# Optimization experiments

Hardware: AMD Instinct MI355X
Metric: run time of the kernel (lower is better)

Reference implementation:

```python
import jax, jax.numpy as jnp
import numpy as np

N_NODES = 50000
N_EDGES = 800000
NFEAT, NHID, NCLASS = 256, 64, 40


def setup_inputs() -> dict:
    key = jax.random.key(0)
    ks = jax.random.split(key, 8)
    x = jax.random.normal(ks[0], (N_NODES, NFEAT), dtype=jnp.float32)
    W1 = jax.random.normal(ks[1], (NFEAT, NHID), dtype=jnp.float32) * (1.0 / np.sqrt(NFEAT))
    b1 = jax.random.normal(ks[2], (NHID,), dtype=jnp.float32) * 0.01
    W2 = jax.random.normal(ks[3], (NHID, NCLASS), dtype=jnp.float32) * (1.0 / np.sqrt(NHID))
    b2 = jax.random.normal(ks[4], (NCLASS,), dtype=jnp.float32) * 0.01
    edge_weight = jax.random.uniform(ks[5], (N_EDGES,), dtype=jnp.float32)
    edge_src = jax.random.randint(ks[6], (N_EDGES,), 0, N_NODES)
    edge_dst = jax.random.randint(ks[7], (N_EDGES,), 0, N_NODES)
    return {"x": x, "W1": W1, "b1": b1, "W2": W2, "b2": b2,
            "edge_weight": edge_weight, "edge_src": edge_src, "edge_dst": edge_dst}


def reference(x, W1, b1, W2, b2, edge_weight, edge_src, edge_dst):
    n = x.shape[0]

    def spmm(h):  # sparse adj @ h via gather + weighted segment-sum
        msgs = h[edge_src] * edge_weight[:, None]  # [E, d]
        return jax.ops.segment_sum(msgs, edge_dst, num_segments=n)

    # gc1: adj @ (x @ W1) + b1, then relu (dropout is identity in eval mode)
    h = jax.nn.relu(spmm(x @ W1) + b1)
    # gc2: adj @ (h @ W2) + b2
    logits = spmm(h @ W2) + b2
    return (logits, jax.nn.log_softmax(logits, axis=1))
```

## Files before the change

### kernel.cpp

```cpp
#include <hip/hip_runtime.h>
#include <math.h>

#define N_NODES 50000
#define N_EDGES 800000
#define NFEAT 256
#define NHID 64
#define NCLASS 40
#define NPB 16
#define NB  3125
#define CAP 512
#define BIN_EPB 8192
#define NBIN 98
#define NGEMM 782
#define ACC2S 68

typedef __attribute__((ext_vector_type(8))) short bf16x8;
typedef __attribute__((ext_vector_type(4))) float f32x4;

__device__ __forceinline__ ushort f2bf(float f) {
    unsigned u = __float_as_uint(f);
    u += 0x7FFF + ((u >> 16) & 1);
    return (ushort)(u >> 16);
}
__device__ __forceinline__ float bf2f(ushort us) {
    return __uint_as_float(((unsigned)us) << 16);
}

__global__ __launch_bounds__(256) void k_prep(const float* __restrict__ W1,
                                              const float* __restrict__ W2,
                                              ushort* __restrict__ W1f,
                                              ushort* __restrict__ W2f) {
    int idx = blockIdx.x * 256 + threadIdx.x;
    if (idx < 2048) {
        int lane = idx & 63, ctks = idx >> 6;
        int ks = ctks & 7, ct = ctks >> 3;
        int col = ct * 16 + (lane & 15);
        int r0 = ks * 32 + (lane >> 4) * 8;
        bf16x8 frag;
        #pragma unroll
        for (int j = 0; j < 8; ++j) frag[j] = (short)f2bf(W1[(r0 + j) * NHID + col]);
        *(bf16x8*)&W1f[(size_t)idx * 8] = frag;
    } else if (idx < 2048 + 384) {
        int i2 = idx - 2048;
        int lane = i2 & 63, ctks = i2 >> 6;
        int ks = ctks & 1, ct = ctks >> 1;
        int col = ct * 16 + (lane & 15);
        int r0 = ks * 32 + (lane >> 4) * 8;
        bf16x8 frag;
        #pragma unroll
        for (int j = 0; j < 8; ++j)
            frag[j] = (short)((col < NCLASS) ? f2bf(W2[(r0 + j) * NCLASS + col]) : 0);
        *(bf16x8*)&W2f[(size_t)i2 * 8] = frag;
    }
}

__global__ __launch_bounds__(1024) void k_mega(const int* __restrict__ esrc,
                                               const int* __restrict__ edst,
                                               const float* __restrict__ ewt,
                                               int* __restrict__ bfill,
                                               int2* __restrict__ binned,
                                               const float* __restrict__ x,
                                               const ushort* __restrict__ W1f,
                                               ushort* __restrict__ xW1b) {
    __shared__ __align__(16) char smem[64 * 256 * 2];
    int tid = threadIdx.x;

    if (blockIdx.x < NBIN) {
        int* lcnt  = (int*)smem;
        int* lbase = lcnt + NB;
        for (int i = tid; i < NB; i += 1024) lcnt[i] = 0;
        __syncthreads();
        int base = blockIdx.x * BIN_EPB;
        #pragma unroll
        for (int k = 0; k < BIN_EPB; k += 1024) {
            int e = base + k + tid;
            if (e < N_EDGES) atomicAdd(&lcnt[edst[e] >> 4], 1);
        }
        __syncthreads();
        for (int i = tid; i < NB; i += 1024) {
            int c = lcnt[i];
            lbase[i] = c ? atomicAdd(&bfill[i], c) : 0;
            lcnt[i] = 0;
        }
        __syncthreads();
        #pragma unroll
        for (int k = 0; k < BIN_EPB; k += 1024) {
            int e = base + k + tid;
            if (e < N_EDGES) {
                int d = edst[e];
                int b = d >> 4;
                int pos = b * CAP + lbase[b] + atomicAdd(&lcnt[b], 1);
                binned[pos] = make_int2(esrc[e] | ((d & 15) << 16),
                                        __float_as_int(ewt[e]));
            }
        }
        return;
    }

    ushort* sX = (ushort*)smem;
    int w = tid >> 6, lane = tid & 63;
    int ct = w & 3, rg = w >> 2;
    int row0 = (blockIdx.x - NBIN) * 64;

    bf16x8 Bf[8];
    #pragma unroll
    for (int ks = 0; ks < 8; ++ks)
        Bf[ks] = *(const bf16x8*)&W1f[(size_t)((ct * 8 + ks) * 64 + lane) * 8];

    {
        int row = tid & 63;
        int colbase = (tid >> 6) * 16;
        int crow = min(row0 + row, N_NODES - 1);
        const float* xp = x + (size_t)crow * NFEAT + colbase;
        #pragma unroll
        for (int c2 = 0; c2 < 2; ++c2) {
            float4 v0 = *(const float4*)(xp + c2 * 8);
            float4 v1 = *(const float4*)(xp + c2 * 8 + 4);
            bf16x8 fr;
            fr[0] = (short)f2bf(v0.x); fr[1] = (short)f2bf(v0.y);
            fr[2] = (short)f2bf(v0.z); fr[3] = (short)f2bf(v0.w);
            fr[4] = (short)f2bf(v1.x); fr[5] = (short)f2bf(v1.y);
            fr[6] = (short)f2bf(v1.z); fr[7] = (short)f2bf(v1.w);
            int chunk = colbase / 8 + c2;
            *(bf16x8*)&sX[row * 256 + ((chunk ^ (row & 7)) * 8)] = fr;
        }
    }
    __syncthreads();

    f32x4 acc = {0.f, 0.f, 0.f, 0.f};
    int arow = rg * 16 + (lane & 15);
    #pragma unroll
    for (int ks = 0; ks < 8; ++ks) {
        int chunk = ks * 4 + (lane >> 4);
        bf16x8 Af = *(const bf16x8*)&sX[arow * 256 + ((chunk ^ (arow & 7)) * 8)];
        acc = __builtin_amdgcn_mfma_f32_16x16x32_bf16(Af, Bf[ks], acc, 0, 0, 0);
    }
    int col = ct * 16 + (lane & 15);
    int rbase = row0 + rg * 16 + (lane >> 4) * 4;
    #pragma unroll
    for (int r = 0; r < 4; ++r) {
        int row = rbase + r;
        if (row < N_NODES)
            xW1b[(size_t)row * NHID + col] = f2bf(acc[r]);
    }
}

__global__ __launch_bounds__(256) void k_spmm1b(const ushort* __restrict__ xW1b,
                                                const int* __restrict__ bfill,
                                                const int2* __restrict__ binned,
                                                const float* __restrict__ b1,
                                                ushort* __restrict__ h_b) {
    __shared__ float accs[4][NPB * NHID];
    int wv = threadIdx.x >> 6, lane = threadIdx.x & 63;
    int b = blockIdx.x;
    float* acc = accs[wv];
    #pragma unroll
    for (int n = 0; n < NPB; ++n) acc[n * NHID + lane] = 0.f;

    int s = b * CAP, e = s + bfill[b];
    int len = e - s;
    int q = (len + 3) >> 2;
    int j = s + wv * q;
    int je = min(j + q, e);
    for (; j + 8 <= je; j += 8) {
        int2 p[8];
        #pragma unroll
        for (int k = 0; k < 8; ++k) p[k] = binned[j + k];
        float g[8];
        #pragma unroll
        for (int k = 0; k < 8; ++k)
            g[k] = bf2f(xW1b[(p[k].x & 0xFFFF) * NHID + lane]);
        #pragma unroll
        for (int k = 0; k < 8; ++k)
            acc[(p[k].x >> 16) * NHID + lane] += __int_as_float(p[k].y) * g[k];
    }
    for (; j < je; ++j) {
        int2 p0 = binned[j];
        float g0 = bf2f(xW1b[(p0.x & 0xFFFF) * NHID + lane]);
        acc[(p0.x >> 16) * NHID + lane] += __int_as_float(p0.y) * g0;
    }
    __syncthreads();

    float bias = b1[lane];
    #pragma unroll
    for (int i = 0; i < 4; ++i) {
        int n = wv * 4 + i;
        float v = accs[0][n * NHID + lane] + accs[1][n * NHID + lane]
                + accs[2][n * NHID + lane] + accs[3][n * NHID + lane] + bias;
        h_b[(size_t)(b * NPB + n) * NHID + lane] = f2bf(v > 0.f ? v : 0.f);
    }
}

__global__ __launch_bounds__(256) void k_spmm2f(const ushort* __restrict__ h_b,
                                                const int* __restrict__ bfill,
                                                const int2* __restrict__ binned,
                                                const ushort* __restrict__ W2f,
                                                const float* __restrict__ b2,
                                                float* __restrict__ out) {
    __shared__ float accs[4][NPB * ACC2S];
    int wv = threadIdx.x >> 6, lane = threadIdx.x & 63;
    int b = blockIdx.x;
    float* acc = accs[wv];
    #pragma unroll
    for (int n = 0; n < NPB; ++n) acc[n * ACC2S + lane] = 0.f;

    int s = b * CAP, e = s + bfill[b];
    int len = e - s;
    int q = (len + 3) >> 2;
    int j = s + wv * q;
    int je = min(j + q, e);
    for (; j + 8 <= je; j += 8) {
        int2 p[8];
        #pragma unroll
        for (int k = 0; k < 8; ++k) p[k] = binned[j + k];
        float g[8];
        #pragma unroll
        for (int k = 0; k < 8; ++k)
            g[k] = bf2f(h_b[(p[k].x & 0xFFFF) * NHID + lane]);
        #pragma unroll
        for (int k = 0; k < 8; ++k)
            acc[(p[k].x >> 16) * ACC2S + lane] += __int_as_float(p[k].y) * g[k];
    }
    for (; j < je; ++j) {
        int2 p0 = binned[j];
        float g0 = bf2f(h_b[(p0.x & 0xFFFF) * NHID + lane]);
        acc[(p0.x >> 16) * ACC2S + lane] += __int_as_float(p0.y) * g0;
    }
    __syncthreads();

    for (int i = threadIdx.x; i < NPB * 64; i += 256) {
        int idx = (i >> 6) * ACC2S + (i & 63);
        accs[0][idx] = accs[0][idx] + accs[1][idx] + accs[2][idx] + accs[3][idx];
    }
    __syncthreads();
    if (wv != 0) return;

    bf16x8 Af[2];
    #pragma unroll
    for (int ks = 0; ks < 2; ++ks) {
        const float* ap = &accs[0][(lane & 15) * ACC2S + ks * 32 + (lane >> 4) * 8];
        #pragma unroll
        for (int jj = 0; jj < 8; ++jj) Af[ks][jj] = (short)f2bf(ap[jj]);
    }
    f32x4 cv[3] = {{0.f,0.f,0.f,0.f},{0.f,0.f,0.f,0.f},{0.f,0.f,0.f,0.f}};
    #pragma unroll
    for (int ct = 0; ct < 3; ++ct) {
        #pragma unroll
        for (int ks = 0; ks < 2; ++ks) {
            bf16x8 Bf = *(const bf16x8*)&W2f[(size_t)((ct * 2 + ks) * 64 + lane) * 8];
            cv[ct] = __builtin_amdgcn_mfma_f32_16x16x32_bf16(Af[ks], Bf, cv[ct], 0, 0, 0);
        }
    }
    int colg = lane & 15;
    int g = lane >> 4;
    float bc0 = b2[colg];
    float bc1 = b2[16 + colg];
    float bc2 = (colg < 8) ? b2[32 + colg] : 0.f;
    #pragma unroll
    for (int i = 0; i < 4; ++i) {
        int node = b * NPB + g * 4 + i;
        float v0 = cv[0][i] + bc0;
        float v1 = cv[1][i] + bc1;
        float v2 = (colg < 8) ? (cv[2][i] + bc2) : -INFINITY;
        float m = fmaxf(fmaxf(v0, v1), v2);
        #pragma unroll
        for (int off = 1; off < 16; off <<= 1) m = fmaxf(m, __shfl_xor(m, off));
        float ex = __expf(v0 - m) + __expf(v1 - m) + ((colg < 8) ? __expf(v2 - m) : 0.f);
        #pragma unroll
        for (int off = 1; off < 16; off <<= 1) ex += __shfl_xor(ex, off);
        float ls = __logf(ex) + m;
        float* o0 = out + (size_t)node * NCLASS;
        float* o1 = o0 + (size_t)N_NODES * NCLASS;
        o0[colg] = v0;            o1[colg] = v0 - ls;
        o0[16 + colg] = v1;       o1[16 + colg] = v1 - ls;
        if (colg < 8) { o0[32 + colg] = v2;  o1[32 + colg] = v2 - ls; }
    }
}


extern "C" void kernel_launch(void* const* d_in, const int* in_sizes, int n_in,
                              void* d_out, int out_size, void* d_ws, size_t ws_size,
                              hipStream_t stream) {
    const float* x    = (const float*)d_in[0];
    const float* W1   = (const float*)d_in[1];
    const float* b1   = (const float*)d_in[2];
    const float* W2   = (const float*)d_in[3];
    const float* b2   = (const float*)d_in[4];
    const float* ewt  = (const float*)d_in[5];
    const int*   esrc = (const int*)d_in[6];
    const int*   edst = (const int*)d_in[7];
    float* out = (float*)d_out;

    char* p = (char*)d_ws;
    ushort* xW1b = (ushort*)p;   p += (size_t)N_NODES * NHID * 2;
    ushort* h_b  = (ushort*)p;   p += (size_t)N_NODES * NHID * 2;
    int2*   binned = (int2*)p;   p += (size_t)NB * CAP * 8;
    ushort* W1f  = (ushort*)p;   p += 2048 * 8 * 2;
    ushort* W2f  = (ushort*)p;   p += 384 * 8 * 2;
    int* bfill   = (int*)p;      p += NB * 4;

    hipMemsetAsync(bfill, 0, NB * sizeof(int), stream);

    k_prep<<<10, 256, 0, stream>>>(W1, W2, W1f, W2f);
    k_mega<<<NBIN + NGEMM, 1024, 0, stream>>>(esrc, edst, ewt, bfill, binned,
                                              x, W1f, xW1b);
    k_spmm1b<<<NB, 256, 0, stream>>>(xW1b, bfill, binned, b1, h_b);
    k_spmm2f<<<NB, 256, 0, stream>>>(h_b, bfill, binned, W2f, b2, out);
}
```

Before: 197.8 us.

## Split edge binning into two-pass coarse then fine radix bucketing

Edge binning by destination now runs in two passes. The first pass scatters edges into 98 coarse buckets of 512 nodes each, so per-block atomics land on few counters and writes go to few regions. A new kernel then splits each coarse bucket into 32 fine 16-node bins. This is meant to cut scattered global writes and global atomic contention from the single-pass scatter into 3125 bins, at the cost of an extra launch and another read and write of all edges.

Measured after the change: 189.4 us. 4.2% less time.

```diff
diff --git a/kernel.cpp b/kernel.cpp
--- a/kernel.cpp
+++ b/kernel.cpp
@@ -9,6 +9,8 @@
 #define NPB 16
 #define NB  3125
 #define CAP 512
+#define NC 98
+#define CAPC 16384
 #define BIN_EPB 8192
 #define NBIN 98
 #define NGEMM 782
@@ -57,8 +59,8 @@
 __global__ __launch_bounds__(1024) void k_mega(const int* __restrict__ esrc,
                                                const int* __restrict__ edst,
                                                const float* __restrict__ ewt,
-                                               int* __restrict__ bfill,
-                                               int2* __restrict__ binned,
+                                               int* __restrict__ bfillc,
+                                               int2* __restrict__ coarse,
                                                const float* __restrict__ x,
                                                const ushort* __restrict__ W1f,
                                                ushort* __restrict__ xW1b) {
@@ -66,32 +68,32 @@
     int tid = threadIdx.x;
 
     if (blockIdx.x < NBIN) {
-        int* lcnt  = (int*)smem;
-        int* lbase = lcnt + NB;
-        for (int i = tid; i < NB; i += 1024) lcnt[i] = 0;
+        int* cnt  = (int*)smem;
+        int* base = cnt + NC;
+        for (int i = tid; i < NC; i += 1024) cnt[i] = 0;
         __syncthreads();
-        int base = blockIdx.x * BIN_EPB;
+        int eb = blockIdx.x * BIN_EPB;
         #pragma unroll
         for (int k = 0; k < BIN_EPB; k += 1024) {
-            int e = base + k + tid;
-            if (e < N_EDGES) atomicAdd(&lcnt[edst[e] >> 4], 1);
+            int e = eb + k + tid;
+            if (e < N_EDGES) atomicAdd(&cnt[edst[e] >> 9], 1);
         }
         __syncthreads();
-        for (int i = tid; i < NB; i += 1024) {
-            int c = lcnt[i];
-            lbase[i] = c ? atomicAdd(&bfill[i], c) : 0;
-            lcnt[i] = 0;
+        for (int i = tid; i < NC; i += 1024) {
+            int c = cnt[i];
+            base[i] = c ? atomicAdd(&bfillc[i], c) : 0;
+            cnt[i] = 0;
         }
         __syncthreads();
         #pragma unroll
         for (int k = 0; k < BIN_EPB; k += 1024) {
-            int e = base + k + tid;
+            int e = eb + k + tid;
             if (e < N_EDGES) {
                 int d = edst[e];
-                int b = d >> 4;
-                int pos = b * CAP + lbase[b] + atomicAdd(&lcnt[b], 1);
-                binned[pos] = make_int2(esrc[e] | ((d & 15) << 16),
-                                        __float_as_int(ewt[e]));
+                int c = d >> 9;
+                int pos = base[c] + atomicAdd(&cnt[c], 1);
+                coarse[(size_t)c * CAPC + pos] =
+                    make_int2(esrc[e] | ((d & 511) << 16), __float_as_int(ewt[e]));
             }
         }
         return;
@@ -142,6 +144,43 @@
         int row = rbase + r;
         if (row < N_NODES)
             xW1b[(size_t)row * NHID + col] = f2bf(acc[r]);
+    }
+}
+
+__global__ __launch_bounds__(512) void k_passB(const int* __restrict__ bfillc,
+                                               const int2* __restrict__ coarse,
+                                               int* __restrict__ bfill,
+                                               int2* __restrict__ binned) {
+    __shared__ int cnt[32];
+    __shared__ int base[32];
+    int tid = threadIdx.x;
+    int c = blockIdx.x >> 1;
+    int half = blockIdx.x & 1;
+    int fillc = bfillc[c];
+    int h0 = (fillc + 1) >> 1;
+    int js = c * CAPC + half * h0;
+    int je = c * CAPC + (half ? fillc : h0);
+
+    if (tid < 32) cnt[tid] = 0;
+    __syncthreads();
+    for (int j = js + tid; j < je; j += 512) {
+        int dstlow = (coarse[j].x >> 16) & 511;
+        atomicAdd(&cnt[dstlow >> 4], 1);
+    }
+    __syncthreads();
+    if (tid < 32) {
+        int cc = cnt[tid];
+        base[tid] = cc ? atomicAdd(&bfill[c * 32 + tid], cc) : 0;
+        cnt[tid] = 0;
+    }
+    __syncthreads();
+    for (int j = js + tid; j < je; j += 512) {
+        int2 p = coarse[j];
+        int dstlow = (p.x >> 16) & 511;
+        int fb = dstlow >> 4;
+        int pos = base[fb] + atomicAdd(&cnt[fb], 1);
+        binned[(size_t)(c * 32 + fb) * CAP + pos] =
+            make_int2((p.x & 0xFFFF) | ((dstlow & 15) << 16), p.y);
     }
 }
 
@@ -294,16 +333,19 @@
     char* p = (char*)d_ws;
     ushort* xW1b = (ushort*)p;   p += (size_t)N_NODES * NHID * 2;
     ushort* h_b  = (ushort*)p;   p += (size_t)N_NODES * NHID * 2;
-    int2*   binned = (int2*)p;   p += (size_t)NB * CAP * 8;
+    int2*   binned = (int2*)p;   p += (size_t)NB * CAP * 8 + 64;
+    int2*   coarse = (int2*)p;   p += (size_t)NC * CAPC * 8;
     ushort* W1f  = (ushort*)p;   p += 2048 * 8 * 2;
     ushort* W2f  = (ushort*)p;   p += 384 * 8 * 2;
+    int* bfillc  = (int*)p;      p += NC * 4;
     int* bfill   = (int*)p;      p += NB * 4;
 
-    hipMemsetAsync(bfill, 0, NB * sizeof(int), stream);
+    hipMemsetAsync(bfillc, 0, (NC + NB) * sizeof(int), stream);
 
     k_prep<<<10, 256, 0, stream>>>(W1, W2, W1f, W2f);
-    k_mega<<<NBIN + NGEMM, 1024, 0, stream>>>(esrc, edst, ewt, bfill, binned,
+    k_mega<<<NBIN + NGEMM, 1024, 0, stream>>>(esrc, edst, ewt, bfillc, coarse,
                                               x, W1f, xW1b);
+    k_passB<<<NC * 2, 512, 0, stream>>>(bfillc, coarse, bfill, binned);
     k_spmm1b<<<NB, 256, 0, stream>>>(xW1b, bfill, binned, b1, h_b);
     k_spmm2f<<<NB, 256, 0, stream>>>(h_b, bfill, binned, W2f, b2, out);
 }
```
